# Kernel tuning notes

Measured on AMD Instinct MI355X. Metric: run time of the kernel, lower is better.

The kernel has to match this reference:

```python
import jax, jax.numpy as jnp
import numpy as np

# Faithful notes on the original torch code:
# - MLP path with n_networks=1: angles = MLP(coeffs), shape [N,1]. Dropout is
#   eval-mode identity (dropout=0.0).
# - aggregate_k_hop: step_k is a single buffer that torch_scatter ACCUMULATES into
#   across hops (scatter(..., out=step_k) adds into out), and enhanced_angles
#   ALIASES angles, so `enhanced_angles += step_k` mutates the angle vector that
#   is read at the next hop. We reproduce both behaviors.
# - k-hop paths are deduplicated via np.unique, i.e. the scatter at hop k sums
#   angles[dest] over UNIQUE (src,dest) pairs reachable in exactly k edge steps.
#   That is exactly the boolean k-th power of the adjacency matrix, so we use
#   dense boolean matrix powers (static shapes, jit-friendly) instead of the
#   dynamic-shape unique() roundtrip.

N_NODES = 4096
IN_DIM = 128
N_EDGES = 131072
K_HOPS = 3


def setup_inputs() -> dict:
    key = jax.random.key(0)
    ks = jax.random.split(key, 8)
    coeffs = jax.random.normal(ks[0], (N_NODES, IN_DIM), dtype=jnp.float32)
    edge_index = jax.random.randint(ks[1], (2, N_EDGES), 0, N_NODES, dtype=jnp.int64)
    # Xavier-normal linear weights (torch layout: [out, in])
    def xavier(k, out_d, in_d):
        std = np.sqrt(2.0 / (in_d + out_d)).astype(np.float32)
        return jax.random.normal(k, (out_d, in_d), dtype=jnp.float32) * std
    W0 = xavier(ks[2], IN_DIM, IN_DIM)
    b0 = jnp.zeros((IN_DIM,), jnp.float32)
    W1 = xavier(ks[3], IN_DIM, IN_DIM)  # use_bias=False
    W2 = xavier(ks[4], IN_DIM, IN_DIM)
    W3 = xavier(ks[5], 1, IN_DIM)
    b3 = jnp.zeros((1,), jnp.float32)
    return {"coeffs": coeffs, "edge_index": edge_index,
            "W0": W0, "b0": b0, "W1": W1, "W2": W2, "W3": W3, "b3": b3}


def reference(coeffs, edge_index, W0, b0, W1, W2, W3, b3):
    n = coeffs.shape[0]
    h = jax.nn.relu(coeffs @ W0.T + b0)
    h = jax.nn.relu(h @ W1.T)
    h = jax.nn.relu(h @ W2.T)
    a = h @ W3.T + b3  # [N, 1]

    # ---- aggregate_k_hop (k=3), f(k) = log(k+1) ----
    row, col = edge_index[0], edge_index[1]
    # hop 1: raw edge list scatter (duplicates kept, as in the original)
    step = jax.ops.segment_sum(a[col] * jnp.float32(np.log(2.0)), row,
                               num_segments=n)  # [N,1]
    a = a + step
    # hops >= 2: unique k-step paths == boolean adjacency power
    A = jnp.zeros((n, n), jnp.bool_).at[row, col].set(True)
    Af = A.astype(jnp.float32)
    Ak = Af
    for k_ in range(2, K_HOPS + 1):
        Ak = ((Ak @ Af) > 0).astype(jnp.float32)  # unique k_-hop reachability
        step = step + jnp.float32(np.log(k_ + 1.0)) * (Ak @ a)
        a = a + step
    return a
```

## Files before the change

### kernel.cpp

```cpp
#include <hip/hip_runtime.h>
#include <cstdint>
#include <cstddef>


constexpr int NN   = 4096;
constexpr int D    = 128;
constexpr int NE   = 131072;
constexpr int WPR  = 64;
constexpr int MAXN = 256;

typedef __attribute__((ext_vector_type(8))) short  short8;
typedef __attribute__((ext_vector_type(4))) float  float4v;

__device__ __forceinline__ unsigned short f32_bf16(float x) {
  unsigned u = __float_as_uint(x);
  return (unsigned short)((u + 0x7FFFu + ((u >> 16) & 1u)) >> 16);
}
__device__ __forceinline__ float bf16_f32(unsigned short b) {
  return __uint_as_float(((unsigned)b) << 16);
}

struct Frag { short8 hi; short8 lo; };

__device__ __forceinline__ Frag mk_frag(float4v a, float4v b) {
  Frag f;
#pragma unroll
  for (int j = 0; j < 4; ++j) {
    float x = a[j];
    unsigned short h = f32_bf16(x);
    f.hi[j] = (short)h;
    f.lo[j] = (short)f32_bf16(x - bf16_f32(h));
    float y = b[j];
    unsigned short h2 = f32_bf16(y);
    f.hi[j + 4] = (short)h2;
    f.lo[j + 4] = (short)f32_bf16(y - bf16_f32(h2));
  }
  return f;
}
__device__ __forceinline__ Frag split8(const float* __restrict__ p) {
  return mk_frag(*(const float4v*)p, *(const float4v*)(p + 4));
}

__device__ __forceinline__ float4v mfma3(const Frag& A, const Frag& B, float4v c) {
  c = __builtin_amdgcn_mfma_f32_16x16x32_bf16(A.lo, B.hi, c, 0, 0, 0);
  c = __builtin_amdgcn_mfma_f32_16x16x32_bf16(A.hi, B.lo, c, 0, 0, 0);
  c = __builtin_amdgcn_mfma_f32_16x16x32_bf16(A.hi, B.hi, c, 0, 0, 0);
  return c;
}

__device__ __forceinline__ float wave_sum64(float v) {
#pragma unroll
  for (int off = 32; off >= 1; off >>= 1) v += __shfl_xor(v, off, 64);
  return v;
}

__global__ __launch_bounds__(256) void pack_w(
    const float* __restrict__ W0, const float* __restrict__ W1,
    const float* __restrict__ W2, short* __restrict__ Wp) {
  int tid = blockIdx.x * 256 + threadIdx.x;
  int lane = tid & 63, kt = (tid >> 6) & 3, o = (tid >> 8) & 7, L = tid >> 11;
  int quad = lane >> 4, l16 = lane & 15;
  const float* W = (L == 0) ? W0 : (L == 1) ? W1 : W2;
  Frag f = split8(W + (size_t)(o * 16 + l16) * D + kt * 32 + quad * 8);
  short* base = Wp + (size_t)(((L * 8 + o) * 4) + kt) * 1024;
  *(short8*)(base + lane * 8) = f.hi;
  *(short8*)(base + 512 + lane * 8) = f.lo;
}

__global__ __launch_bounds__(256, 2) void mlp_mfma(
    const float* __restrict__ coeffs, const short* __restrict__ Wp,
    const float* __restrict__ b0,
    const float* __restrict__ W3, const float* __restrict__ b3,
    float* __restrict__ a0v,
    unsigned long long* __restrict__ A, float* __restrict__ s1) {
  __shared__ float hbuf[16 * 132];
  __shared__ float psh[4][16];
  const int b = blockIdx.x, t = threadIdx.x;
  const int wave = t >> 6, lane = t & 63;
  const int quad = lane >> 4, l16 = lane & 15;
  const int node0 = b * 8;
  const int ot0 = 2 * wave, ot1 = 2 * wave + 1;

  {
    float4v z4 = {0.f, 0.f, 0.f, 0.f};
    ((float4v*)A)[(size_t)b * 256 + t] = z4;
    if (t < 2) ((float4v*)(s1 + node0))[t] = z4;
  }

  float4v r0, r1;
#pragma unroll
  for (int L = 0; L < 3; ++L) {
    const short* WL = Wp + (size_t)L * 32768;
    short8 Bf[4][4];
#pragma unroll
    for (int kt = 0; kt < 4; ++kt) {
      const short* p0 = WL + (size_t)(ot0 * 4 + kt) * 1024 + lane * 8;
      const short* p1 = WL + (size_t)(ot1 * 4 + kt) * 1024 + lane * 8;
      Bf[kt][0] = *(const short8*)p0;
      Bf[kt][1] = *(const short8*)(p0 + 512);
      Bf[kt][2] = *(const short8*)p1;
      Bf[kt][3] = *(const short8*)(p1 + 512);
    }
    Frag Af[4];
    if (L == 0) {
      const float* abase = coeffs + (size_t)(node0 + (l16 & 7)) * D + quad * 8;
      float4v araw[8];
#pragma unroll
      for (int kt = 0; kt < 4; ++kt) {
        araw[2 * kt]     = *(const float4v*)(abase + kt * 32);
        araw[2 * kt + 1] = *(const float4v*)(abase + kt * 32 + 4);
      }
#pragma unroll
      for (int kt = 0; kt < 4; ++kt) Af[kt] = mk_frag(araw[2 * kt], araw[2 * kt + 1]);
    } else {
      const float* abase = hbuf + (l16 & 7) * 132 + quad * 8;
#pragma unroll
      for (int kt = 0; kt < 4; ++kt) Af[kt] = split8(abase + kt * 32);
    }
    float4v acc0 = {0.f, 0.f, 0.f, 0.f}, acc1 = acc0;
#pragma unroll
    for (int kt = 0; kt < 4; ++kt) {
      Frag B0; B0.hi = Bf[kt][0]; B0.lo = Bf[kt][1];
      Frag B1; B1.hi = Bf[kt][2]; B1.lo = Bf[kt][3];
      acc0 = mfma3(Af[kt], B0, acc0);
      acc1 = mfma3(Af[kt], B1, acc1);
    }
    if (L == 0) {
      float ba = b0[ot0 * 16 + l16], bb = b0[ot1 * 16 + l16];
#pragma unroll
      for (int j = 0; j < 4; ++j) { acc0[j] += ba; acc1[j] += bb; }
    }
#pragma unroll
    for (int j = 0; j < 4; ++j) {
      acc0[j] = fmaxf(acc0[j], 0.f);
      acc1[j] = fmaxf(acc1[j], 0.f);
    }
    if (L < 2) {
      __syncthreads();
#pragma unroll
      for (int j = 0; j < 4; ++j) {
        hbuf[(quad * 4 + j) * 132 + ot0 * 16 + l16] = acc0[j];
        hbuf[(quad * 4 + j) * 132 + ot1 * 16 + l16] = acc1[j];
      }
      __syncthreads();
    } else {
      r0 = acc0; r1 = acc1;
    }
  }
  float w3a = W3[ot0 * 16 + l16], w3b = W3[ot1 * 16 + l16];
#pragma unroll
  for (int j = 0; j < 4; ++j) {
    float v = fmaf(r0[j], w3a, r1[j] * w3b);
#pragma unroll
    for (int off = 1; off <= 8; off <<= 1) v += __shfl_xor(v, off, 64);
    if (l16 == 0) psh[wave][quad * 4 + j] = v;
  }
  __syncthreads();
  if (t < 8)
    a0v[node0 + t] = psh[0][t] + psh[1][t] + psh[2][t] + psh[3][t] + b3[0];
}

__global__ __launch_bounds__(256) void build_graph(
    const int* __restrict__ er, const int* __restrict__ ec,
    const float* __restrict__ a0, unsigned long long* __restrict__ A,
    float* __restrict__ s1) {
  int e = blockIdx.x * 256 + threadIdx.x;
  if (e >= NE) return;
  int r = er[e] & (NN - 1);
  int c = ec[e] & (NN - 1);
  atomicOr(&A[(size_t)r * WPR + (c >> 6)], 1ull << (c & 63));
  atomicAdd(&s1[r], a0[c] * 0.6931471805599453f);
}

__device__ __forceinline__ unsigned long long gather_row(
    const unsigned long long* __restrict__ Arow,
    const unsigned long long* __restrict__ SRC,
    int i, int lane, unsigned short* __restrict__ nbr, int* __restrict__ ncnt) {
  if (lane == 0) *ncnt = 0;
  unsigned long long rw = Arow[(size_t)i * WPR + lane];
  int c = __popcll(rw);
  int base = 0;
  if (c) base = atomicAdd(ncnt, c);
  while (rw) {
    int b = __builtin_ctzll(rw);
    rw &= rw - 1ull;
    if (base < MAXN) nbr[base] = (unsigned short)((lane << 6) + b);
    ++base;
  }
  int cnt = *ncnt;
  cnt = cnt < MAXN ? cnt : MAXN;
  unsigned long long acc = 0ull;
  int j = 0;
  for (; j + 8 <= cnt; j += 8) {
    unsigned long long v0 = SRC[(size_t)nbr[j + 0] * WPR + lane];
    unsigned long long v1 = SRC[(size_t)nbr[j + 1] * WPR + lane];
    unsigned long long v2 = SRC[(size_t)nbr[j + 2] * WPR + lane];
    unsigned long long v3 = SRC[(size_t)nbr[j + 3] * WPR + lane];
    unsigned long long v4 = SRC[(size_t)nbr[j + 4] * WPR + lane];
    unsigned long long v5 = SRC[(size_t)nbr[j + 5] * WPR + lane];
    unsigned long long v6 = SRC[(size_t)nbr[j + 6] * WPR + lane];
    unsigned long long v7 = SRC[(size_t)nbr[j + 7] * WPR + lane];
    acc |= ((v0 | v1) | (v2 | v3)) | ((v4 | v5) | (v6 | v7));
  }
  for (; j < cnt; ++j) acc |= SRC[(size_t)nbr[j] * WPR + lane];
  return acc;
}

__device__ __forceinline__ float masked_dot(
    unsigned long long m, const float* __restrict__ vl,
    const float* __restrict__ wsum, int lane) {
  int cnt = __popcll(m);
  bool inv = cnt > 32;
  unsigned long long it = inv ? ~m : m;
  float part = inv ? wsum[lane] : 0.f;
  float sgn = inv ? -1.f : 1.f;
  const float* p = vl + lane * 65;
  float acc = 0.f;
  while (it) {
    int b = __builtin_ctzll(it);
    it &= it - 1ull;
    acc += p[b];
  }
  return fmaf(sgn, acc, part);
}

__device__ __forceinline__ void word_sums(const float* __restrict__ vl,
                                          float* __restrict__ wsm, int t) {
  if (t < 64) {
    float s = 0.f;
    const float* p = vl + t * 65;
#pragma unroll 16
    for (int b2 = 0; b2 < 64; ++b2) s += p[b2];
    wsm[t] = s;
  }
}

__global__ __launch_bounds__(256) void hop2(
    const unsigned long long* __restrict__ A, unsigned long long* __restrict__ A2,
    const float* __restrict__ a0, const float* __restrict__ s1,
    float* __restrict__ s2, float* __restrict__ a2) {
  __shared__ float vl[64 * 65];
  __shared__ float wsm[64];
  __shared__ unsigned short nbr[4][MAXN];
  __shared__ int ncnt[4];
  int t = threadIdx.x, wave = t >> 6, lane = t & 63;
#pragma unroll
  for (int u = 0; u < 16; ++u) {
    int j = t + u * 256;
    vl[(j >> 6) * 65 + (j & 63)] = a0[j] + s1[j];
  }
  __syncthreads();
  word_sums(vl, wsm, t);
  __syncthreads();
  int i = blockIdx.x * 4 + wave;
  unsigned long long acc = gather_row(A, A, i, lane, nbr[wave], &ncnt[wave]);
  A2[(size_t)i * WPR + lane] = acc;
  float part = masked_dot(acc, vl, wsm, lane);
  part = wave_sum64(part);
  if (lane == 0) {
    float s2v = fmaf(1.0986122886681098f, part, s1[i]);
    s2[i] = s2v;
    a2[i] = vl[(i >> 6) * 65 + (i & 63)] + s2v;
  }
}

__global__ __launch_bounds__(256) void hop3(
    const unsigned long long* __restrict__ A, const unsigned long long* __restrict__ A2,
    const float* __restrict__ a2, const float* __restrict__ s2,
    float* __restrict__ out) {
  __shared__ float vl[64 * 65];
  __shared__ float wsm[64];
  __shared__ unsigned short nbr[4][MAXN];
  __shared__ int ncnt[4];
  int t = threadIdx.x, wave = t >> 6, lane = t & 63;
#pragma unroll
  for (int u = 0; u < 16; ++u) {
    int j = t + u * 256;
    vl[(j >> 6) * 65 + (j & 63)] = a2[j];
  }
  __syncthreads();
  word_sums(vl, wsm, t);
  __syncthreads();
  int i = blockIdx.x * 4 + wave;
  unsigned long long acc = gather_row(A, A2, i, lane, nbr[wave], &ncnt[wave]);
  float part = masked_dot(acc, vl, wsm, lane);
  part = wave_sum64(part);
  if (lane == 0)
    out[i] = vl[(i >> 6) * 65 + (i & 63)] +
             fmaf(1.3862943611198906f, part, s2[i]);
}

extern "C" void kernel_launch(void* const* d_in, const int* in_sizes, int n_in,
                              void* d_out, int out_size, void* d_ws, size_t ws_size,
                              hipStream_t stream) {
  const float* coeffs = (const float*)d_in[0];
  const int*   edge   = (const int*)d_in[1];
  const float* W0 = (const float*)d_in[2];
  const float* b0 = (const float*)d_in[3];
  const float* W1 = (const float*)d_in[4];
  const float* W2 = (const float*)d_in[5];
  const float* W3 = (const float*)d_in[6];
  const float* b3 = (const float*)d_in[7];
  float* out = (float*)d_out;

  char* ws = (char*)d_ws;
  unsigned long long* A  = (unsigned long long*)ws;
  unsigned long long* A2 = (unsigned long long*)(ws + (2u << 20));
  float* f   = (float*)(ws + (4u << 20));
  float* a0v = f;
  float* s1  = f + 4096;
  float* s2  = f + 8192;
  float* a2v = f + 12288;
  short* Wp  = (short*)(ws + (4u << 20) + 128 * 1024);

  pack_w<<<24, 256, 0, stream>>>(W0, W1, W2, Wp);
  mlp_mfma<<<NN / 8, 256, 0, stream>>>(coeffs, Wp, b0, W3, b3, a0v, A, s1);
  build_graph<<<NE / 256, 256, 0, stream>>>(edge, edge + NE, a0v, A, s1);
  hop2<<<NN / 4, 256, 0, stream>>>(A, A2, a0v, s1, s2, a2v);
  hop3<<<NN / 4, 256, 0, stream>>>(A, A2, a2v, s2, out);
}
```

Measured before the change: 117.5 us.

## Process two rows per wave in hop kernels, move zeroing, vectorize edge loads

Each wave in the hop2/hop3 kernels now handles two adjacency rows, interleaving their neighbour gathers so more independent memory loads are in flight. The block count is halved and the per-row neighbour list cap drops from 256 to 128. Word sums are spread across all four waves, zeroing of A and s1 moves into the small pack_w kernel, and build_graph loads two edges per thread as int2. The lower neighbour cap truncates rows with more than 128 neighbours; with about 32 random edges per row, that cap is assumed never to be reached.

```diff
diff --git a/kernel.cpp b/kernel.cpp
--- a/kernel.cpp
+++ b/kernel.cpp
@@ -7,10 +7,11 @@
 constexpr int D    = 128;
 constexpr int NE   = 131072;
 constexpr int WPR  = 64;
-constexpr int MAXN = 256;
+constexpr int MAXN = 128;
 
 typedef __attribute__((ext_vector_type(8))) short  short8;
 typedef __attribute__((ext_vector_type(4))) float  float4v;
+typedef unsigned long long u64;
 
 __device__ __forceinline__ unsigned short f32_bf16(float x) {
   unsigned u = __float_as_uint(x);
@@ -56,7 +57,8 @@
 
 __global__ __launch_bounds__(256) void pack_w(
     const float* __restrict__ W0, const float* __restrict__ W1,
-    const float* __restrict__ W2, short* __restrict__ Wp) {
+    const float* __restrict__ W2, short* __restrict__ Wp,
+    float4v* __restrict__ Az, float4v* __restrict__ s1z) {
   int tid = blockIdx.x * 256 + threadIdx.x;
   int lane = tid & 63, kt = (tid >> 6) & 3, o = (tid >> 8) & 7, L = tid >> 11;
   int quad = lane >> 4, l16 = lane & 15;
@@ -65,14 +67,20 @@
   short* base = Wp + (size_t)(((L * 8 + o) * 4) + kt) * 1024;
   *(short8*)(base + lane * 8) = f.hi;
   *(short8*)(base + 512 + lane * 8) = f.lo;
+  float4v z4 = {0.f, 0.f, 0.f, 0.f};
+#pragma unroll
+  for (int r = 0; r < 22; ++r) {
+    int j = tid + r * 6144;
+    if (j < 131072) Az[j] = z4;
+  }
+  if (tid < 1024) s1z[tid] = z4;
 }
 
 __global__ __launch_bounds__(256, 2) void mlp_mfma(
     const float* __restrict__ coeffs, const short* __restrict__ Wp,
     const float* __restrict__ b0,
     const float* __restrict__ W3, const float* __restrict__ b3,
-    float* __restrict__ a0v,
-    unsigned long long* __restrict__ A, float* __restrict__ s1) {
+    float* __restrict__ a0v) {
   __shared__ float hbuf[16 * 132];
   __shared__ float psh[4][16];
   const int b = blockIdx.x, t = threadIdx.x;
@@ -81,12 +89,6 @@
   const int node0 = b * 8;
   const int ot0 = 2 * wave, ot1 = 2 * wave + 1;
 
-  {
-    float4v z4 = {0.f, 0.f, 0.f, 0.f};
-    ((float4v*)A)[(size_t)b * 256 + t] = z4;
-    if (t < 2) ((float4v*)(s1 + node0))[t] = z4;
-  }
-
   float4v r0, r1;
 #pragma unroll
   for (int L = 0; L < 3; ++L) {
@@ -162,22 +164,25 @@
 
 __global__ __launch_bounds__(256) void build_graph(
     const int* __restrict__ er, const int* __restrict__ ec,
-    const float* __restrict__ a0, unsigned long long* __restrict__ A,
+    const float* __restrict__ a0, u64* __restrict__ A,
     float* __restrict__ s1) {
-  int e = blockIdx.x * 256 + threadIdx.x;
-  if (e >= NE) return;
-  int r = er[e] & (NN - 1);
-  int c = ec[e] & (NN - 1);
-  atomicOr(&A[(size_t)r * WPR + (c >> 6)], 1ull << (c & 63));
-  atomicAdd(&s1[r], a0[c] * 0.6931471805599453f);
-}
-
-__device__ __forceinline__ unsigned long long gather_row(
-    const unsigned long long* __restrict__ Arow,
-    const unsigned long long* __restrict__ SRC,
-    int i, int lane, unsigned short* __restrict__ nbr, int* __restrict__ ncnt) {
+  int e2 = blockIdx.x * 256 + threadIdx.x;
+  int2 r2 = ((const int2*)er)[e2];
+  int2 c2 = ((const int2*)ec)[e2];
+#pragma unroll
+  for (int u = 0; u < 2; ++u) {
+    int r = (u ? r2.y : r2.x) & (NN - 1);
+    int c = (u ? c2.y : c2.x) & (NN - 1);
+    atomicOr(&A[(size_t)r * WPR + (c >> 6)], 1ull << (c & 63));
+    atomicAdd(&s1[r], a0[c] * 0.6931471805599453f);
+  }
+}
+
+__device__ __forceinline__ int compact_row(
+    const u64* __restrict__ Arow, int i, int lane,
+    unsigned short* __restrict__ nbr, int* __restrict__ ncnt) {
   if (lane == 0) *ncnt = 0;
-  unsigned long long rw = Arow[(size_t)i * WPR + lane];
+  u64 rw = Arow[(size_t)i * WPR + lane];
   int c = __popcll(rw);
   int base = 0;
   if (c) base = atomicAdd(ncnt, c);
@@ -188,30 +193,41 @@
     ++base;
   }
   int cnt = *ncnt;
-  cnt = cnt < MAXN ? cnt : MAXN;
-  unsigned long long acc = 0ull;
-  int j = 0;
-  for (; j + 8 <= cnt; j += 8) {
-    unsigned long long v0 = SRC[(size_t)nbr[j + 0] * WPR + lane];
-    unsigned long long v1 = SRC[(size_t)nbr[j + 1] * WPR + lane];
-    unsigned long long v2 = SRC[(size_t)nbr[j + 2] * WPR + lane];
-    unsigned long long v3 = SRC[(size_t)nbr[j + 3] * WPR + lane];
-    unsigned long long v4 = SRC[(size_t)nbr[j + 4] * WPR + lane];
-    unsigned long long v5 = SRC[(size_t)nbr[j + 5] * WPR + lane];
-    unsigned long long v6 = SRC[(size_t)nbr[j + 6] * WPR + lane];
-    unsigned long long v7 = SRC[(size_t)nbr[j + 7] * WPR + lane];
-    acc |= ((v0 | v1) | (v2 | v3)) | ((v4 | v5) | (v6 | v7));
-  }
-  for (; j < cnt; ++j) acc |= SRC[(size_t)nbr[j] * WPR + lane];
-  return acc;
+  return cnt < MAXN ? cnt : MAXN;
+}
+
+#define GATHER4(acc, lst, j)                                   \
+  {                                                            \
+    u64 g0 = SRC[(size_t)lst[j + 0] * WPR + lane];             \
+    u64 g1 = SRC[(size_t)lst[j + 1] * WPR + lane];             \
+    u64 g2 = SRC[(size_t)lst[j + 2] * WPR + lane];             \
+    u64 g3 = SRC[(size_t)lst[j + 3] * WPR + lane];             \
+    acc |= (g0 | g1) | (g2 | g3);                              \
+  }
+
+__device__ __forceinline__ void gather2(
+    const u64* __restrict__ SRC, int lane,
+    const unsigned short* __restrict__ na, int ca,
+    const unsigned short* __restrict__ nb, int cb,
+    u64& accA, u64& accB) {
+  accA = 0ull; accB = 0ull;
+  int ja = 0, jb = 0;
+  for (; ja + 4 <= ca && jb + 4 <= cb; ja += 4, jb += 4) {
+    GATHER4(accA, na, ja)
+    GATHER4(accB, nb, jb)
+  }
+  for (; ja + 4 <= ca; ja += 4) GATHER4(accA, na, ja)
+  for (; jb + 4 <= cb; jb += 4) GATHER4(accB, nb, jb)
+  for (; ja < ca; ++ja) accA |= SRC[(size_t)na[ja] * WPR + lane];
+  for (; jb < cb; ++jb) accB |= SRC[(size_t)nb[jb] * WPR + lane];
 }
 
 __device__ __forceinline__ float masked_dot(
-    unsigned long long m, const float* __restrict__ vl,
+    u64 m, const float* __restrict__ vl,
     const float* __restrict__ wsum, int lane) {
   int cnt = __popcll(m);
   bool inv = cnt > 32;
-  unsigned long long it = inv ? ~m : m;
+  u64 it = inv ? ~m : m;
   float part = inv ? wsum[lane] : 0.f;
   float sgn = inv ? -1.f : 1.f;
   const float* p = vl + lane * 65;
@@ -225,24 +241,27 @@
 }
 
 __device__ __forceinline__ void word_sums(const float* __restrict__ vl,
-                                          float* __restrict__ wsm, int t) {
-  if (t < 64) {
-    float s = 0.f;
-    const float* p = vl + t * 65;
-#pragma unroll 16
-    for (int b2 = 0; b2 < 64; ++b2) s += p[b2];
-    wsm[t] = s;
-  }
+                                          float* __restrict__ psum,
+                                          float* __restrict__ wsm,
+                                          int wave, int lane, int t) {
+  float s = 0.f;
+  const float* p = vl + lane * 65 + wave * 16;
+#pragma unroll
+  for (int b = 0; b < 16; ++b) s += p[b];
+  psum[wave * 64 + lane] = s;
+  __syncthreads();
+  if (t < 64) wsm[t] = psum[t] + psum[64 + t] + psum[128 + t] + psum[192 + t];
 }
 
 __global__ __launch_bounds__(256) void hop2(
-    const unsigned long long* __restrict__ A, unsigned long long* __restrict__ A2,
+    const u64* __restrict__ A, u64* __restrict__ A2,
     const float* __restrict__ a0, const float* __restrict__ s1,
     float* __restrict__ s2, float* __restrict__ a2) {
   __shared__ float vl[64 * 65];
+  __shared__ float psum[256];
   __shared__ float wsm[64];
-  __shared__ unsigned short nbr[4][MAXN];
-  __shared__ int ncnt[4];
+  __shared__ unsigned short nbr[8][MAXN];
+  __shared__ int ncnt[8];
   int t = threadIdx.x, wave = t >> 6, lane = t & 63;
 #pragma unroll
   for (int u = 0; u < 16; ++u) {
@@ -250,28 +269,36 @@
     vl[(j >> 6) * 65 + (j & 63)] = a0[j] + s1[j];
   }
   __syncthreads();
-  word_sums(vl, wsm, t);
-  __syncthreads();
-  int i = blockIdx.x * 4 + wave;
-  unsigned long long acc = gather_row(A, A, i, lane, nbr[wave], &ncnt[wave]);
-  A2[(size_t)i * WPR + lane] = acc;
-  float part = masked_dot(acc, vl, wsm, lane);
-  part = wave_sum64(part);
+  word_sums(vl, psum, wsm, wave, lane, t);
+  __syncthreads();
+  int ia = blockIdx.x * 8 + wave * 2, ib = ia + 1;
+  int ca = compact_row(A, ia, lane, nbr[wave * 2], &ncnt[wave * 2]);
+  int cb = compact_row(A, ib, lane, nbr[wave * 2 + 1], &ncnt[wave * 2 + 1]);
+  u64 accA, accB;
+  gather2(A, lane, nbr[wave * 2], ca, nbr[wave * 2 + 1], cb, accA, accB);
+  A2[(size_t)ia * WPR + lane] = accA;
+  A2[(size_t)ib * WPR + lane] = accB;
+  float pa = wave_sum64(masked_dot(accA, vl, wsm, lane));
+  float pb = wave_sum64(masked_dot(accB, vl, wsm, lane));
   if (lane == 0) {
-    float s2v = fmaf(1.0986122886681098f, part, s1[i]);
-    s2[i] = s2v;
-    a2[i] = vl[(i >> 6) * 65 + (i & 63)] + s2v;
+    float s2a = fmaf(1.0986122886681098f, pa, s1[ia]);
+    s2[ia] = s2a;
+    a2[ia] = vl[(ia >> 6) * 65 + (ia & 63)] + s2a;
+    float s2b = fmaf(1.0986122886681098f, pb, s1[ib]);
+    s2[ib] = s2b;
+    a2[ib] = vl[(ib >> 6) * 65 + (ib & 63)] + s2b;
   }
 }
 
 __global__ __launch_bounds__(256) void hop3(
-    const unsigned long long* __restrict__ A, const unsigned long long* __restrict__ A2,
+    const u64* __restrict__ A, const u64* __restrict__ A2,
     const float* __restrict__ a2, const float* __restrict__ s2,
     float* __restrict__ out) {
   __shared__ float vl[64 * 65];
+  __shared__ float psum[256];
   __shared__ float wsm[64];
-  __shared__ unsigned short nbr[4][MAXN];
-  __shared__ int ncnt[4];
+  __shared__ unsigned short nbr[8][MAXN];
+  __shared__ int ncnt[8];
   int t = threadIdx.x, wave = t >> 6, lane = t & 63;
 #pragma unroll
   for (int u = 0; u < 16; ++u) {
@@ -279,15 +306,21 @@
     vl[(j >> 6) * 65 + (j & 63)] = a2[j];
   }
   __syncthreads();
-  word_sums(vl, wsm, t);
-  __syncthreads();
-  int i = blockIdx.x * 4 + wave;
-  unsigned long long acc = gather_row(A, A2, i, lane, nbr[wave], &ncnt[wave]);
-  float part = masked_dot(acc, vl, wsm, lane);
-  part = wave_sum64(part);
-  if (lane == 0)
-    out[i] = vl[(i >> 6) * 65 + (i & 63)] +
-             fmaf(1.3862943611198906f, part, s2[i]);
+  word_sums(vl, psum, wsm, wave, lane, t);
+  __syncthreads();
+  int ia = blockIdx.x * 8 + wave * 2, ib = ia + 1;
+  int ca = compact_row(A, ia, lane, nbr[wave * 2], &ncnt[wave * 2]);
+  int cb = compact_row(A, ib, lane, nbr[wave * 2 + 1], &ncnt[wave * 2 + 1]);
+  u64 accA, accB;
+  gather2(A2, lane, nbr[wave * 2], ca, nbr[wave * 2 + 1], cb, accA, accB);
+  float pa = wave_sum64(masked_dot(accA, vl, wsm, lane));
+  float pb = wave_sum64(masked_dot(accB, vl, wsm, lane));
+  if (lane == 0) {
+    out[ia] = vl[(ia >> 6) * 65 + (ia & 63)] +
+              fmaf(1.3862943611198906f, pa, s2[ia]);
+    out[ib] = vl[(ib >> 6) * 65 + (ib & 63)] +
+              fmaf(1.3862943611198906f, pb, s2[ib]);
+  }
 }
 
 extern "C" void kernel_launch(void* const* d_in, const int* in_sizes, int n_in,
@@ -304,8 +337,8 @@
   float* out = (float*)d_out;
 
   char* ws = (char*)d_ws;
-  unsigned long long* A  = (unsigned long long*)ws;
-  unsigned long long* A2 = (unsigned long long*)(ws + (2u << 20));
+  u64* A  = (u64*)ws;
+  u64* A2 = (u64*)(ws + (2u << 20));
   float* f   = (float*)(ws + (4u << 20));
   float* a0v = f;
   float* s1  = f + 4096;
@@ -313,9 +346,9 @@
   float* a2v = f + 12288;
   short* Wp  = (short*)(ws + (4u << 20) + 128 * 1024);
 
-  pack_w<<<24, 256, 0, stream>>>(W0, W1, W2, Wp);
-  mlp_mfma<<<NN / 8, 256, 0, stream>>>(coeffs, Wp, b0, W3, b3, a0v, A, s1);
-  build_graph<<<NE / 256, 256, 0, stream>>>(edge, edge + NE, a0v, A, s1);
-  hop2<<<NN / 4, 256, 0, stream>>>(A, A2, a0v, s1, s2, a2v);
-  hop3<<<NN / 4, 256, 0, stream>>>(A, A2, a2v, s2, out);
-}
+  pack_w<<<24, 256, 0, stream>>>(W0, W1, W2, Wp, (float4v*)A, (float4v*)s1);
+  mlp_mfma<<<NN / 8, 256, 0, stream>>>(coeffs, Wp, b0, W3, b3, a0v);
+  build_graph<<<NE / 512, 256, 0, stream>>>(edge, edge + NE, a0v, A, s1);
+  hop2<<<NN / 8, 256, 0, stream>>>(A, A2, a0v, s1, s2, a2v);
+  hop3<<<NN / 8, 256, 0, stream>>>(A, A2, a2v, s2, out);
+}
```

New measurement: 120.6 us. 2.6% more time.
